# Performance work log

Measured on AMD Instinct MI355X. Metric: run time of the kernel, lower is better.

## Reference

```python
import jax, jax.numpy as jnp
import numpy as np

N_NODES = 50000
N_EDGES = 800000
IN_CH = 256
OUT_CH = 64
ALPHA = 0.2  # leaky relu slope
NEG_BIG = -9e15


def setup_inputs() -> dict:
    key = jax.random.key(0)
    k1, k2, k3, k4 = jax.random.split(key, 4)
    x = jax.random.normal(k1, (N_NODES, IN_CH), dtype=jnp.float32)
    edge_index = jax.random.randint(k2, (2, N_EDGES), 0, N_NODES, dtype=jnp.int64)
    # xavier-uniform-ish params
    W = jax.random.normal(k3, (IN_CH, OUT_CH), dtype=jnp.float32) * (1.414 * np.sqrt(2.0 / (IN_CH + OUT_CH)))
    a = jax.random.normal(k4, (1, 2 * OUT_CH), dtype=jnp.float32) * (1.414 * np.sqrt(2.0 / (1 + 2 * OUT_CH)))
    return {"x": x, "edge_index": edge_index, "W": W, "a": a}


def reference(x, edge_index, W, a):
    wh = x @ W                                  # [N, F]
    src, dst = edge_index[0], edge_index[1]     # [E], [E]
    F_out = wh.shape[1]
    # (a * [wh_src, wh_dst]).sum(1) == wh_src @ a_src + wh_dst @ a_dst; compute per-node then gather
    e_src = wh @ a[0, :F_out]                   # [N]
    e_dst = wh @ a[0, F_out:]                   # [N]
    e = jax.nn.leaky_relu(e_src[src] + e_dst[dst], ALPHA)[:, None]  # [E, 1]
    e = jnp.where(e > 0, e, jnp.float32(NEG_BIG))
    attention = jax.nn.softmax(e, axis=0)       # global softmax over ALL edges (faithful to source)
    msgs = attention * wh[src]                  # [E, F]
    h_prime = jax.ops.segment_sum(msgs, dst, num_segments=wh.shape[0])  # [N, F]
    return jax.nn.elu(h_prime)
```

## Files before the change

kernel.cpp:

```cpp
#include <hip/hip_runtime.h>
#include <hip/hip_bf16.h>

#define N_NODES 50000
#define N_EDGES 800000
#define IN_CH 256
#define OUT_CH 64
#define NEG_BIG -9e15f
#define NBLK_E 3125
#define NBLK_N 196

typedef __bf16 bfvec8 __attribute__((ext_vector_type(8)));
typedef float floatx4 __attribute__((ext_vector_type(4)));

#define WS_WHB   0
#define WS_W32   6400000
#define WS_PSRC  9600000
#define WS_SRC16 11200000
#define WS_DST16 12800000
#define WS_CNT   14400000
#define WS_ROWP  14600000
#define WS_WOFS  14800000
#define WS_WTH   15000000
#define WS_WTL   15040000
#define WS_ESRC  15080000
#define WS_EDST  15280000
#define WS_BMAX  15480000
#define WS_BSUM  15496000
#define WS_BTOT  15512000
#define WS_BBASE 15513000
#define WS_M     15514000
#define WS_Z     15514004
#define WS_FLAGS 15514008

__device__ __forceinline__ float loadf(const void* p, size_t i, int isf32) {
    return isf32 ? ((const float*)p)[i]
                 : __bfloat162float(((const __hip_bfloat16*)p)[i]);
}
__device__ __forceinline__ void load_edge(const int* __restrict__ ei, int i, int f64,
                                          int& s, int& d) {
    if (f64) {
        int2 ps = ((const int2*)ei)[i];
        int2 pd = ((const int2*)ei)[N_EDGES + i];
        s = ps.x; d = pd.x;
    } else {
        s = ei[i]; d = ei[N_EDGES + i];
    }
    s = min(max(s, 0), N_NODES - 1);
    d = min(max(d, 0), N_NODES - 1);
}

__global__ __launch_bounds__(256) void k_flags(const int* __restrict__ ei,
                                               const unsigned* __restrict__ xw,
                                               int* __restrict__ flags) {
    int t = threadIdx.x;
    int v = 0;
    for (int i = t; i < 2048; i += 256) v |= ei[2 * i + 1];
    unsigned lo = xw[t] & 0xFFFFu;
    unsigned e8 = (lo >> 7) & 0xFFu;
    int hit = (e8 >= 96u && e8 <= 144u) ? 1 : 0;
#pragma unroll
    for (int off = 32; off > 0; off >>= 1) {
        v |= __shfl_down(v, off);
        hit += __shfl_down(hit, off);
    }
    __shared__ int sv[4], sh[4];
    if ((t & 63) == 0) { sv[t >> 6] = v; sh[t >> 6] = hit; }
    __syncthreads();
    if (t == 0) {
        flags[0] = ((sv[0] | sv[1] | sv[2] | sv[3]) == 0) ? 1 : 0;
        flags[1] = ((sh[0] + sh[1] + sh[2] + sh[3]) < 192) ? 1 : 0;
    }
}

__global__ __launch_bounds__(256) void k_prep(const void* __restrict__ Wv,
                                              const int* __restrict__ flags,
                                              __bf16* __restrict__ Wth,
                                              __bf16* __restrict__ Wtl) {
    int isf = flags[1];
    int t = blockIdx.x * 256 + threadIdx.x;
    int c = t >> 8, k = t & 255;
    float w = loadf(Wv, (size_t)k * OUT_CH + c, isf);
    __bf16 h = (__bf16)w;
    Wth[t] = h;
    Wtl[t] = (__bf16)(w - (float)h);
}

__global__ __launch_bounds__(256, 2) void k_mm(const void* __restrict__ xv,
                                               const __bf16* __restrict__ Wth,
                                               const __bf16* __restrict__ Wtl,
                                               const void* __restrict__ av,
                                               const int* __restrict__ flags,
                                               __bf16* __restrict__ whb,
                                               float* __restrict__ esrc,
                                               float* __restrict__ edst) {
    __shared__ __bf16 lW[2][64 * 256];
    int tid = threadIdx.x;
    int isf = flags[1];
    int gw = (blockIdx.x * 256 + tid) >> 6;
    int lane = tid & 63;
    int m = lane & 15, quad = lane >> 4;
    int nb = gw * 16;
    bool active = gw < N_NODES / 16;

    floatx4 x0[8], x1[8];
    bfvec8 xa[8];
    if (active) {
        if (isf) {
            const float* xr = (const float*)xv + (size_t)(nb + m) * IN_CH + quad * 8;
#pragma unroll
            for (int s = 0; s < 8; ++s) {
                x0[s] = *(const floatx4*)(xr + s * 32);
                x1[s] = *(const floatx4*)(xr + s * 32 + 4);
            }
        } else {
            const __bf16* xr = (const __bf16*)xv + (size_t)(nb + m) * IN_CH + quad * 8;
#pragma unroll
            for (int s = 0; s < 8; ++s) xa[s] = *(const bfvec8*)(xr + s * 32);
        }
    }

#pragma unroll
    for (int i = 0; i < 8; ++i) {
        int f = i * 256 + tid;
        int r = f >> 5, c = f & 31;
        int cs = c ^ (r & 31);
        *(bfvec8*)(&lW[0][r * 256 + cs * 8]) = *(const bfvec8*)(Wth + r * 256 + c * 8);
        *(bfvec8*)(&lW[1][r * 256 + cs * 8]) = *(const bfvec8*)(Wtl + r * 256 + c * 8);
    }
    __syncthreads();

    if (!active) return;

    floatx4 acc[4];
#pragma unroll
    for (int ct = 0; ct < 4; ++ct) acc[ct] = (floatx4){0.f, 0.f, 0.f, 0.f};

    if (isf) {
#pragma unroll
        for (int s = 0; s < 8; ++s) {
            float v[8];
            *(floatx4*)(v)     = x0[s];
            *(floatx4*)(v + 4) = x1[s];
            bfvec8 ahi, alo;
#pragma unroll
            for (int j = 0; j < 8; ++j) {
                __bf16 h = (__bf16)v[j];
                ahi[j] = h;
                alo[j] = (__bf16)(v[j] - (float)h);
            }
#pragma unroll
            for (int ct = 0; ct < 4; ++ct) {
                int row = ct * 16 + m;
                int cs = ((s * 4 + quad) ^ (row & 31)) * 8;
                bfvec8 bhi = *(const bfvec8*)(&lW[0][row * 256 + cs]);
                bfvec8 blo = *(const bfvec8*)(&lW[1][row * 256 + cs]);
                acc[ct] = __builtin_amdgcn_mfma_f32_16x16x32_bf16(ahi, blo, acc[ct], 0, 0, 0);
                acc[ct] = __builtin_amdgcn_mfma_f32_16x16x32_bf16(alo, bhi, acc[ct], 0, 0, 0);
                acc[ct] = __builtin_amdgcn_mfma_f32_16x16x32_bf16(ahi, bhi, acc[ct], 0, 0, 0);
            }
        }
    } else {
#pragma unroll
        for (int s = 0; s < 8; ++s) {
#pragma unroll
            for (int ct = 0; ct < 4; ++ct) {
                int row = ct * 16 + m;
                int cs = ((s * 4 + quad) ^ (row & 31)) * 8;
                bfvec8 bhi = *(const bfvec8*)(&lW[0][row * 256 + cs]);
                bfvec8 blo = *(const bfvec8*)(&lW[1][row * 256 + cs]);
                acc[ct] = __builtin_amdgcn_mfma_f32_16x16x32_bf16(xa[s], blo, acc[ct], 0, 0, 0);
                acc[ct] = __builtin_amdgcn_mfma_f32_16x16x32_bf16(xa[s], bhi, acc[ct], 0, 0, 0);
            }
        }
    }

    float a1[4], a2[4];
#pragma unroll
    for (int ct = 0; ct < 4; ++ct) {
        a1[ct] = loadf(av, ct * 16 + m, isf);
        a2[ct] = loadf(av, OUT_CH + ct * 16 + m, isf);
    }
#pragma unroll
    for (int r = 0; r < 4; ++r) {
        int node = nb + quad * 4 + r;
        float s1 = 0.f, s2 = 0.f;
#pragma unroll
        for (int ct = 0; ct < 4; ++ct) {
            float vv = acc[ct][r];
            whb[(size_t)node * OUT_CH + ct * 16 + m] = (__bf16)vv;
            s1 += vv * a1[ct];
            s2 += vv * a2[ct];
        }
#pragma unroll
        for (int off = 1; off < 16; off <<= 1) {
            s1 += __shfl_xor(s1, off);
            s2 += __shfl_xor(s2, off);
        }
        if (m == 0) { esrc[node] = s1; edst[node] = s2; }
    }
}

__global__ __launch_bounds__(256) void k_edge(const int* __restrict__ ei,
                                              const int* __restrict__ flags,
                                              const float* __restrict__ esrc,
                                              const float* __restrict__ edst,
                                              unsigned short* __restrict__ src16,
                                              unsigned short* __restrict__ dst16,
                                              int* __restrict__ cnt,
                                              float* __restrict__ bmax) {
    int f64 = flags[0];
    int i = blockIdx.x * 256 + threadIdx.x;
    int s, d;
    load_edge(ei, i, f64, s, d);
    src16[i] = (unsigned short)s;
    dst16[i] = (unsigned short)d;
    float v = esrc[s] + edst[d];
    float ev = v > 0.0f ? v : NEG_BIG;
    if (v > 0.0f) atomicAdd(&cnt[d], 1);
    float mx = ev;
#pragma unroll
    for (int off = 32; off > 0; off >>= 1) mx = fmaxf(mx, __shfl_down(mx, off));
    __shared__ float sm[4];
    if ((threadIdx.x & 63) == 0) sm[threadIdx.x >> 6] = mx;
    __syncthreads();
    if (threadIdx.x == 0)
        bmax[blockIdx.x] = fmaxf(fmaxf(sm[0], sm[1]), fmaxf(sm[2], sm[3]));
}

__global__ __launch_bounds__(256) void k_scanA(const int* __restrict__ cnt,
                                               int* __restrict__ rowptr,
                                               int* __restrict__ btot) {
    int t = threadIdx.x, lane = t & 63, wid = t >> 6;
    int idx = blockIdx.x * 256 + t;
    int v = (idx < N_NODES) ? cnt[idx] : 0;
    int incl = v;
#pragma unroll
    for (int off = 1; off < 64; off <<= 1) {
        int u = __shfl_up(incl, off);
        if (lane >= off) incl += u;
    }
    __shared__ int wsum[4];
    if (lane == 63) wsum[wid] = incl;
    __syncthreads();
    int wbase = 0;
#pragma unroll
    for (int w = 0; w < 4; ++w) if (w < wid) wbase += wsum[w];
    if (idx < N_NODES) rowptr[idx] = wbase + incl - v;
    if (t == 255) btot[blockIdx.x] = wbase + incl;
}

__global__ __launch_bounds__(256) void k_scanB(const int* __restrict__ btot,
                                               int* __restrict__ bbase,
                                               const float* __restrict__ bmax,
                                               float* __restrict__ M) {
    int t = threadIdx.x, lane = t & 63, wid = t >> 6;
    float mx = NEG_BIG;
    for (int i = t; i < NBLK_E; i += 256) mx = fmaxf(mx, bmax[i]);
#pragma unroll
    for (int off = 32; off > 0; off >>= 1) mx = fmaxf(mx, __shfl_down(mx, off));
    __shared__ float smax[4];
    if (lane == 0) smax[wid] = mx;

    int v = (t < NBLK_N) ? btot[t] : 0;
    int incl = v;
#pragma unroll
    for (int off = 1; off < 64; off <<= 1) {
        int u = __shfl_up(incl, off);
        if (lane >= off) incl += u;
    }
    __shared__ int wsum[4];
    if (lane == 63) wsum[wid] = incl;
    __syncthreads();
    int wbase = 0;
#pragma unroll
    for (int w = 0; w < 4; ++w) if (w < wid) wbase += wsum[w];
    if (t < NBLK_N) bbase[t] = wbase + incl - v;
    if (t == 0) *M = fmaxf(fmaxf(smax[0], smax[1]), fmaxf(smax[2], smax[3]));
}

__global__ __launch_bounds__(256) void k_scanC(int* __restrict__ rowptr,
                                               int* __restrict__ wofs,
                                               const int* __restrict__ bbase) {
    int idx = blockIdx.x * 256 + threadIdx.x;
    if (idx < N_NODES) {
        int r = rowptr[idx] + bbase[blockIdx.x];
        rowptr[idx] = r;
        wofs[idx] = r;
    }
}

__global__ __launch_bounds__(256) void k_exp(const float* __restrict__ Mp,
                                             const float* __restrict__ esrc,
                                             const float* __restrict__ edst,
                                             const unsigned short* __restrict__ src16,
                                             const unsigned short* __restrict__ dst16,
                                             int* __restrict__ wofs,
                                             float* __restrict__ w32,
                                             unsigned short* __restrict__ psrc,
                                             float* __restrict__ bsum) {
    float M = *Mp;
    int i = blockIdx.x * 256 + threadIdx.x;
    int s = src16[i], d = dst16[i];
    float v = esrc[s] + edst[d];
    float ev = v > 0.0f ? v : NEG_BIG;
    float t = expf(ev - M);
    if (v > 0.0f) {
        int pos = atomicAdd(&wofs[d], 1);
        w32[pos] = t;
        psrc[pos] = (unsigned short)s;
    }
#pragma unroll
    for (int off = 32; off > 0; off >>= 1) t += __shfl_down(t, off);
    __shared__ float sm[4];
    if ((threadIdx.x & 63) == 0) sm[threadIdx.x >> 6] = t;
    __syncthreads();
    if (threadIdx.x == 0) bsum[blockIdx.x] = sm[0] + sm[1] + sm[2] + sm[3];
}

__global__ __launch_bounds__(256) void k_rsum(const float* __restrict__ bsum,
                                              float* __restrict__ Z) {
    float s = 0.0f;
    for (int i = threadIdx.x; i < NBLK_E; i += 256) s += bsum[i];
#pragma unroll
    for (int off = 32; off > 0; off >>= 1) s += __shfl_down(s, off);
    __shared__ float sm[4];
    if ((threadIdx.x & 63) == 0) sm[threadIdx.x >> 6] = s;
    __syncthreads();
    if (threadIdx.x == 0) *Z = sm[0] + sm[1] + sm[2] + sm[3];
}

__global__ __launch_bounds__(256) void k_gather(const int* __restrict__ rowptr,
                                                const int* __restrict__ wofs,
                                                const float* __restrict__ w32,
                                                const unsigned short* __restrict__ psrc,
                                                const __bf16* __restrict__ whb,
                                                const float* __restrict__ Zp,
                                                float* __restrict__ out) {
    int gw = (blockIdx.x * 256 + (int)threadIdx.x) >> 6;
    int lane = threadIdx.x & 63;
    int sub = lane >> 3;
    int cg  = lane & 7;
    int beg = rowptr[gw];
    int end = wofs[gw];
    float Z = *Zp;
    float invZ = (Z > 0.0f) ? 1.0f / Z : 0.0f;

    float acc[8];
#pragma unroll
    for (int k = 0; k < 8; ++k) acc[k] = 0.0f;

    for (int j0 = beg; j0 < end; j0 += 8) {
        int j = j0 + sub;
        bool valid = j < end;
        int jj = valid ? j : beg;
        float t = valid ? w32[jj] : 0.0f;
        int s = psrc[jj];
        bfvec8 v = *(const bfvec8*)(whb + (size_t)s * OUT_CH + cg * 8);
#pragma unroll
        for (int k = 0; k < 8; ++k) acc[k] += t * (float)v[k];
    }

#pragma unroll
    for (int mask = 8; mask <= 32; mask <<= 1) {
#pragma unroll
        for (int k = 0; k < 8; ++k) acc[k] += __shfl_xor(acc[k], mask);
    }

    if (sub == 0) {
        floatx4 o0, o1;
#pragma unroll
        for (int k = 0; k < 4; ++k) {
            float h = acc[k] * invZ;
            o0[k] = h > 0.0f ? h : expf(h) - 1.0f;
        }
#pragma unroll
        for (int k = 0; k < 4; ++k) {
            float h = acc[4 + k] * invZ;
            o1[k] = h > 0.0f ? h : expf(h) - 1.0f;
        }
        float* dst = out + (size_t)gw * OUT_CH + cg * 8;
        *(floatx4*)(dst)     = o0;
        *(floatx4*)(dst + 4) = o1;
    }
}

extern "C" void kernel_launch(void* const* d_in, const int* in_sizes, int n_in,
                              void* d_out, int out_size, void* d_ws, size_t ws_size,
                              hipStream_t stream) {
    const void* x  = d_in[0];
    const int* ei  = (const int*)d_in[1];
    const void* W  = d_in[2];
    const void* a  = d_in[3];
    float* out     = (float*)d_out;

    char* ws = (char*)d_ws;
    __bf16* whb  = (__bf16*)(ws + WS_WHB);
    float* w32   = (float*)(ws + WS_W32);
    unsigned short* psrc  = (unsigned short*)(ws + WS_PSRC);
    unsigned short* src16 = (unsigned short*)(ws + WS_SRC16);
    unsigned short* dst16 = (unsigned short*)(ws + WS_DST16);
    int* cnt     = (int*)(ws + WS_CNT);
    int* rowptr  = (int*)(ws + WS_ROWP);
    int* wofs    = (int*)(ws + WS_WOFS);
    __bf16* Wth  = (__bf16*)(ws + WS_WTH);
    __bf16* Wtl  = (__bf16*)(ws + WS_WTL);
    float* esrc  = (float*)(ws + WS_ESRC);
    float* edst  = (float*)(ws + WS_EDST);
    float* bmax  = (float*)(ws + WS_BMAX);
    float* bsum  = (float*)(ws + WS_BSUM);
    int*   btot  = (int*)(ws + WS_BTOT);
    int*   bbase = (int*)(ws + WS_BBASE);
    float* M     = (float*)(ws + WS_M);
    float* Z     = (float*)(ws + WS_Z);
    int*   flags = (int*)(ws + WS_FLAGS);

    hipMemsetAsync(cnt, 0, N_NODES * sizeof(int), stream);

    k_flags <<<1,      256, 0, stream>>>(ei, (const unsigned*)x, flags);
    k_prep  <<<64,     256, 0, stream>>>(W, flags, Wth, Wtl);
    k_mm    <<<782,    256, 0, stream>>>(x, Wth, Wtl, a, flags, whb, esrc, edst);
    k_edge  <<<NBLK_E, 256, 0, stream>>>(ei, flags, esrc, edst, src16, dst16, cnt, bmax);
    k_scanA <<<NBLK_N, 256, 0, stream>>>(cnt, rowptr, btot);
    k_scanB <<<1,      256, 0, stream>>>(btot, bbase, bmax, M);
    k_scanC <<<NBLK_N, 256, 0, stream>>>(rowptr, wofs, bbase);
    k_exp   <<<NBLK_E, 256, 0, stream>>>(M, esrc, edst, src16, dst16, wofs, w32, psrc, bsum);
    k_rsum  <<<1,      256, 0, stream>>>(bsum, Z);
    k_gather<<<N_NODES / 4, 256, 0, stream>>>(rowptr, wofs, w32, psrc, whb, Z, out);
}
```

Baseline: 190.8 us.

## Use upper-bound softmax shift from per-node maxima and fuse exp into edge pass

Replaces the exact global max of edge scores with an upper bound max(esrc)+max(edst), computed by atomicMax on order-preserving encoded floats in the matmul kernel. The edge kernel can then evaluate exp directly and emit block sums, so the separate exp kernel's recomputation and the standalone Z-reduction kernel go away. The flags kernel is merged into the W-prep kernel. This removes two launches and one pass over the edge scores, at the cost of an extra per-edge weight buffer and possible underflow if the bound sits far above the true maximum.

```diff
diff --git a/kernel.cpp b/kernel.cpp
--- a/kernel.cpp
+++ b/kernel.cpp
@@ -5,7 +5,6 @@
 #define N_EDGES 800000
 #define IN_CH 256
 #define OUT_CH 64
-#define NEG_BIG -9e15f
 #define NBLK_E 3125
 #define NBLK_N 196
 
@@ -17,21 +16,29 @@
 #define WS_PSRC  9600000
 #define WS_SRC16 11200000
 #define WS_DST16 12800000
-#define WS_CNT   14400000
-#define WS_ROWP  14600000
-#define WS_WOFS  14800000
-#define WS_WTH   15000000
-#define WS_WTL   15040000
-#define WS_ESRC  15080000
-#define WS_EDST  15280000
-#define WS_BMAX  15480000
-#define WS_BSUM  15496000
-#define WS_BTOT  15512000
-#define WS_BBASE 15513000
-#define WS_M     15514000
-#define WS_Z     15514004
-#define WS_FLAGS 15514008
-
+#define WS_WE    14400000
+#define WS_CNT   17600000
+#define WS_KEYS  17800000
+#define WS_ROWP  17800016
+#define WS_WOFS  18000016
+#define WS_WTH   18200016
+#define WS_WTL   18232784
+#define WS_ESRC  18265552
+#define WS_EDST  18465552
+#define WS_BSUM  18665552
+#define WS_BTOT  18678064
+#define WS_BBASE 18678848
+#define WS_Z     18679632
+#define WS_FLAGS 18679636
+
+__device__ __forceinline__ unsigned encode_f(float f) {
+    unsigned u = __float_as_uint(f);
+    return (u & 0x80000000u) ? ~u : (u | 0x80000000u);
+}
+__device__ __forceinline__ float decode_f(unsigned u) {
+    unsigned b = (u & 0x80000000u) ? (u & 0x7fffffffu) : ~u;
+    return __uint_as_float(b);
+}
 __device__ __forceinline__ float loadf(const void* p, size_t i, int isf32) {
     return isf32 ? ((const float*)p)[i]
                  : __bfloat162float(((const __hip_bfloat16*)p)[i]);
@@ -49,9 +56,12 @@
     d = min(max(d, 0), N_NODES - 1);
 }
 
-__global__ __launch_bounds__(256) void k_flags(const int* __restrict__ ei,
-                                               const unsigned* __restrict__ xw,
-                                               int* __restrict__ flags) {
+__global__ __launch_bounds__(256) void k_prep(const void* __restrict__ Wv,
+                                              const int* __restrict__ ei,
+                                              const unsigned* __restrict__ xw,
+                                              int* __restrict__ flags,
+                                              __bf16* __restrict__ Wth,
+                                              __bf16* __restrict__ Wtl) {
     int t = threadIdx.x;
     int v = 0;
     for (int i = t; i < 2048; i += 256) v |= ei[2 * i + 1];
@@ -66,23 +76,23 @@
     __shared__ int sv[4], sh[4];
     if ((t & 63) == 0) { sv[t >> 6] = v; sh[t >> 6] = hit; }
     __syncthreads();
+    __shared__ int s_isf;
     if (t == 0) {
-        flags[0] = ((sv[0] | sv[1] | sv[2] | sv[3]) == 0) ? 1 : 0;
-        flags[1] = ((sh[0] + sh[1] + sh[2] + sh[3]) < 192) ? 1 : 0;
-    }
-}
-
-__global__ __launch_bounds__(256) void k_prep(const void* __restrict__ Wv,
-                                              const int* __restrict__ flags,
-                                              __bf16* __restrict__ Wth,
-                                              __bf16* __restrict__ Wtl) {
-    int isf = flags[1];
-    int t = blockIdx.x * 256 + threadIdx.x;
-    int c = t >> 8, k = t & 255;
+        int f64 = ((sv[0] | sv[1] | sv[2] | sv[3]) == 0) ? 1 : 0;
+        int isf = ((sh[0] + sh[1] + sh[2] + sh[3]) < 192) ? 1 : 0;
+        flags[0] = f64;
+        flags[1] = isf;
+        s_isf = isf;
+    }
+    __syncthreads();
+    int isf = s_isf;
+
+    int g = blockIdx.x * 256 + t;
+    int c = g >> 8, k = g & 255;
     float w = loadf(Wv, (size_t)k * OUT_CH + c, isf);
     __bf16 h = (__bf16)w;
-    Wth[t] = h;
-    Wtl[t] = (__bf16)(w - (float)h);
+    Wth[g] = h;
+    Wtl[g] = (__bf16)(w - (float)h);
 }
 
 __global__ __launch_bounds__(256, 2) void k_mm(const void* __restrict__ xv,
@@ -92,7 +102,8 @@
                                                const int* __restrict__ flags,
                                                __bf16* __restrict__ whb,
                                                float* __restrict__ esrc,
-                                               float* __restrict__ edst) {
+                                               float* __restrict__ edst,
+                                               unsigned* __restrict__ keys) {
     __shared__ __bf16 lW[2][64 * 256];
     int tid = threadIdx.x;
     int isf = flags[1];
@@ -180,6 +191,7 @@
         a1[ct] = loadf(av, ct * 16 + m, isf);
         a2[ct] = loadf(av, OUT_CH + ct * 16 + m, isf);
     }
+    float mS = -3.0e38f, mD = -3.0e38f;
 #pragma unroll
     for (int r = 0; r < 4; ++r) {
         int node = nb + quad * 4 + r;
@@ -197,34 +209,54 @@
             s2 += __shfl_xor(s2, off);
         }
         if (m == 0) { esrc[node] = s1; edst[node] = s2; }
+        mS = fmaxf(mS, s1);
+        mD = fmaxf(mD, s2);
+    }
+#pragma unroll
+    for (int mask = 16; mask <= 32; mask <<= 1) {
+        mS = fmaxf(mS, __shfl_xor(mS, mask));
+        mD = fmaxf(mD, __shfl_xor(mD, mask));
+    }
+    if (lane == 0) {
+        atomicMax(&keys[0], encode_f(mS));
+        atomicMax(&keys[1], encode_f(mD));
     }
 }
 
 __global__ __launch_bounds__(256) void k_edge(const int* __restrict__ ei,
                                               const int* __restrict__ flags,
+                                              const unsigned* __restrict__ keys,
                                               const float* __restrict__ esrc,
                                               const float* __restrict__ edst,
                                               unsigned short* __restrict__ src16,
                                               unsigned short* __restrict__ dst16,
+                                              float* __restrict__ we,
                                               int* __restrict__ cnt,
-                                              float* __restrict__ bmax) {
+                                              float* __restrict__ bsum) {
     int f64 = flags[0];
+    float Mp = decode_f(keys[0]) + decode_f(keys[1]);
     int i = blockIdx.x * 256 + threadIdx.x;
     int s, d;
     load_edge(ei, i, f64, s, d);
     src16[i] = (unsigned short)s;
     dst16[i] = (unsigned short)d;
     float v = esrc[s] + edst[d];
-    float ev = v > 0.0f ? v : NEG_BIG;
-    if (v > 0.0f) atomicAdd(&cnt[d], 1);
-    float mx = ev;
-#pragma unroll
-    for (int off = 32; off > 0; off >>= 1) mx = fmaxf(mx, __shfl_down(mx, off));
+    float w, t;
+    if (v > 0.0f) {
+        w = expf(v - Mp);
+        t = w;
+        atomicAdd(&cnt[d], 1);
+    } else {
+        w = -1.0f;
+        t = 0.0f;
+    }
+    we[i] = w;
+#pragma unroll
+    for (int off = 32; off > 0; off >>= 1) t += __shfl_down(t, off);
     __shared__ float sm[4];
-    if ((threadIdx.x & 63) == 0) sm[threadIdx.x >> 6] = mx;
-    __syncthreads();
-    if (threadIdx.x == 0)
-        bmax[blockIdx.x] = fmaxf(fmaxf(sm[0], sm[1]), fmaxf(sm[2], sm[3]));
+    if ((threadIdx.x & 63) == 0) sm[threadIdx.x >> 6] = t;
+    __syncthreads();
+    if (threadIdx.x == 0) bsum[blockIdx.x] = sm[0] + sm[1] + sm[2] + sm[3];
 }
 
 __global__ __launch_bounds__(256) void k_scanA(const int* __restrict__ cnt,
@@ -251,15 +283,15 @@
 
 __global__ __launch_bounds__(256) void k_scanB(const int* __restrict__ btot,
                                                int* __restrict__ bbase,
-                                               const float* __restrict__ bmax,
-                                               float* __restrict__ M) {
+                                               const float* __restrict__ bsum,
+                                               float* __restrict__ Z) {
     int t = threadIdx.x, lane = t & 63, wid = t >> 6;
-    float mx = NEG_BIG;
-    for (int i = t; i < NBLK_E; i += 256) mx = fmaxf(mx, bmax[i]);
-#pragma unroll
-    for (int off = 32; off > 0; off >>= 1) mx = fmaxf(mx, __shfl_down(mx, off));
-    __shared__ float smax[4];
-    if (lane == 0) smax[wid] = mx;
+    float zs = 0.0f;
+    for (int i = t; i < NBLK_E; i += 256) zs += bsum[i];
+#pragma unroll
+    for (int off = 32; off > 0; off >>= 1) zs += __shfl_down(zs, off);
+    __shared__ float sz[4];
+    if (lane == 0) sz[wid] = zs;
 
     int v = (t < NBLK_N) ? btot[t] : 0;
     int incl = v;
@@ -275,7 +307,7 @@
 #pragma unroll
     for (int w = 0; w < 4; ++w) if (w < wid) wbase += wsum[w];
     if (t < NBLK_N) bbase[t] = wbase + incl - v;
-    if (t == 0) *M = fmaxf(fmaxf(smax[0], smax[1]), fmaxf(smax[2], smax[3]));
+    if (t == 0) *Z = sz[0] + sz[1] + sz[2] + sz[3];
 }
 
 __global__ __launch_bounds__(256) void k_scanC(int* __restrict__ rowptr,
@@ -289,44 +321,20 @@
     }
 }
 
-__global__ __launch_bounds__(256) void k_exp(const float* __restrict__ Mp,
-                                             const float* __restrict__ esrc,
-                                             const float* __restrict__ edst,
-                                             const unsigned short* __restrict__ src16,
-                                             const unsigned short* __restrict__ dst16,
-                                             int* __restrict__ wofs,
-                                             float* __restrict__ w32,
-                                             unsigned short* __restrict__ psrc,
-                                             float* __restrict__ bsum) {
-    float M = *Mp;
+__global__ __launch_bounds__(256) void k_place(const float* __restrict__ we,
+                                               const unsigned short* __restrict__ src16,
+                                               const unsigned short* __restrict__ dst16,
+                                               int* __restrict__ wofs,
+                                               float* __restrict__ w32,
+                                               unsigned short* __restrict__ psrc) {
     int i = blockIdx.x * 256 + threadIdx.x;
-    int s = src16[i], d = dst16[i];
-    float v = esrc[s] + edst[d];
-    float ev = v > 0.0f ? v : NEG_BIG;
-    float t = expf(ev - M);
-    if (v > 0.0f) {
+    float w = we[i];
+    if (w >= 0.0f) {
+        int d = dst16[i];
         int pos = atomicAdd(&wofs[d], 1);
-        w32[pos] = t;
-        psrc[pos] = (unsigned short)s;
-    }
-#pragma unroll
-    for (int off = 32; off > 0; off >>= 1) t += __shfl_down(t, off);
-    __shared__ float sm[4];
-    if ((threadIdx.x & 63) == 0) sm[threadIdx.x >> 6] = t;
-    __syncthreads();
-    if (threadIdx.x == 0) bsum[blockIdx.x] = sm[0] + sm[1] + sm[2] + sm[3];
-}
-
-__global__ __launch_bounds__(256) void k_rsum(const float* __restrict__ bsum,
-                                              float* __restrict__ Z) {
-    float s = 0.0f;
-    for (int i = threadIdx.x; i < NBLK_E; i += 256) s += bsum[i];
-#pragma unroll
-    for (int off = 32; off > 0; off >>= 1) s += __shfl_down(s, off);
-    __shared__ float sm[4];
-    if ((threadIdx.x & 63) == 0) sm[threadIdx.x >> 6] = s;
-    __syncthreads();
-    if (threadIdx.x == 0) *Z = sm[0] + sm[1] + sm[2] + sm[3];
+        w32[pos] = w;
+        psrc[pos] = src16[i];
+    }
 }
 
 __global__ __launch_bounds__(256) void k_gather(const int* __restrict__ rowptr,
@@ -399,31 +407,29 @@
     unsigned short* psrc  = (unsigned short*)(ws + WS_PSRC);
     unsigned short* src16 = (unsigned short*)(ws + WS_SRC16);
     unsigned short* dst16 = (unsigned short*)(ws + WS_DST16);
+    float* we    = (float*)(ws + WS_WE);
     int* cnt     = (int*)(ws + WS_CNT);
+    unsigned* keys = (unsigned*)(ws + WS_KEYS);
     int* rowptr  = (int*)(ws + WS_ROWP);
     int* wofs    = (int*)(ws + WS_WOFS);
     __bf16* Wth  = (__bf16*)(ws + WS_WTH);
     __bf16* Wtl  = (__bf16*)(ws + WS_WTL);
     float* esrc  = (float*)(ws + WS_ESRC);
     float* edst  = (float*)(ws + WS_EDST);
-    float* bmax  = (float*)(ws + WS_BMAX);
     float* bsum  = (float*)(ws + WS_BSUM);
     int*   btot  = (int*)(ws + WS_BTOT);
     int*   bbase = (int*)(ws + WS_BBASE);
-    float* M     = (float*)(ws + WS_M);
     float* Z     = (float*)(ws + WS_Z);
     int*   flags = (int*)(ws + WS_FLAGS);
 
-    hipMemsetAsync(cnt, 0, N_NODES * sizeof(int), stream);
-
-    k_flags <<<1,      256, 0, stream>>>(ei, (const unsigned*)x, flags);
-    k_prep  <<<64,     256, 0, stream>>>(W, flags, Wth, Wtl);
-    k_mm    <<<782,    256, 0, stream>>>(x, Wth, Wtl, a, flags, whb, esrc, edst);
-    k_edge  <<<NBLK_E, 256, 0, stream>>>(ei, flags, esrc, edst, src16, dst16, cnt, bmax);
+    hipMemsetAsync(cnt, 0, N_NODES * sizeof(int) + 8, stream);
+
+    k_prep  <<<64,     256, 0, stream>>>(W, ei, (const unsigned*)x, flags, Wth, Wtl);
+    k_mm    <<<782,    256, 0, stream>>>(x, Wth, Wtl, a, flags, whb, esrc, edst, keys);
+    k_edge  <<<NBLK_E, 256, 0, stream>>>(ei, flags, keys, esrc, edst, src16, dst16, we, cnt, bsum);
     k_scanA <<<NBLK_N, 256, 0, stream>>>(cnt, rowptr, btot);
-    k_scanB <<<1,      256, 0, stream>>>(btot, bbase, bmax, M);
+    k_scanB <<<1,      256, 0, stream>>>(btot, bbase, bsum, Z);
     k_scanC <<<NBLK_N, 256, 0, stream>>>(rowptr, wofs, bbase);
-    k_exp   <<<NBLK_E, 256, 0, stream>>>(M, esrc, edst, src16, dst16, wofs, w32, psrc, bsum);
-    k_rsum  <<<1,      256, 0, stream>>>(bsum, Z);
+    k_place <<<NBLK_E, 256, 0, stream>>>(we, src16, dst16, wofs, w32, psrc);
     k_gather<<<N_NODES / 4, 256, 0, stream>>>(rowptr, wofs, w32, psrc, whb, Z, out);
 }
```

After: 249.6 us. +30.8%, slower.
